# Optimization experiments

Measured on AMD Instinct MI355X. Metric: run time of the kernel, lower is better.

The kernel has to match this reference:

```python
import jax, jax.numpy as jnp
import numpy as np

J6, J3 = 13, 30          # joints with 6-dim and 3-dim outputs (contiguous groups)
J = J6 + J3              # 43 joints total
D = 512                  # latent_dim
B, T = 16, 196


def setup_inputs() -> dict:
    key = jax.random.key(0)
    ks = jax.random.split(key, 7)
    s = 0.02  # weight init scale
    return {
        "x":   jax.random.normal(ks[0], (B, T, J, D), dtype=jnp.float32),
        "W1":  jax.random.normal(ks[1], (J, D, D), dtype=jnp.float32) * s,
        "b1":  jax.random.normal(ks[2], (J, D), dtype=jnp.float32) * s,
        "W2a": jax.random.normal(ks[3], (J6, D, 6), dtype=jnp.float32) * s,
        "b2a": jax.random.normal(ks[4], (J6, 6), dtype=jnp.float32) * s,
        "W2b": jax.random.normal(ks[5], (J3, D, 3), dtype=jnp.float32) * s,
        "b2b": jax.random.normal(ks[6], (J3, 3), dtype=jnp.float32) * s,
    }


def reference(x, W1, b1, W2a, b2a, W2b, b2b):
    # Per-joint MLP: Linear(D,D) -> GELU -> Linear(D,out_dim_j), concatenated
    # over joints along the last dim (heterogeneous 'dk' mode, vectorized).
    h = jnp.einsum('btjd,jde->btje', x, W1) + b1          # [B,T,J,D]
    h = jax.nn.gelu(h, approximate=False)                  # torch nn.GELU (erf)
    oa = jnp.einsum('btjd,jdo->btjo', h[:, :, :J6], W2a) + b2a  # [B,T,13,6]
    ob = jnp.einsum('btjd,jdo->btjo', h[:, :, J6:], W2b) + b2b  # [B,T,30,3]
    b, t = x.shape[0], x.shape[1]
    # torch.cat(out_list, dim=-1) in joint order == group-wise reshape + concat
    motion = jnp.concatenate([oa.reshape(b, t, -1), ob.reshape(b, t, -1)], axis=-1)
    return motion  # [B, T, 13*6 + 30*3] = [B, T, 168]
```

## Files before the change

kernel.cpp:

```cpp
#include <hip/hip_runtime.h>

typedef unsigned short ushort_t;
typedef short short8 __attribute__((ext_vector_type(8)));
typedef float f32x4 __attribute__((ext_vector_type(4)));

#define J_TOT 43
#define J6 13
#define D_DIM 512
#define BT 3136
#define OUTW 168
#define MTILES 49
#define NWG (MTILES * J_TOT)

__device__ __forceinline__ unsigned short bf16rne(float f) {
    unsigned u = __builtin_bit_cast(unsigned, f);
    u += 0x7fffu + ((u >> 16) & 1u);
    return (unsigned short)(u >> 16);
}

__device__ __forceinline__ float gelu_f(float v) {
    float t = v * __builtin_fmaf(v * v, 0.0356774081f, 0.7978845608f);
    float e = __builtin_amdgcn_exp2f(t * 2.8853900818f);
    float s = __builtin_amdgcn_rcpf(1.0f + e);
    return __builtin_fmaf(-v, s, v);
}

__device__ __forceinline__ void async_ld16(const void* gsrc, void* ldst) {
    __builtin_amdgcn_global_load_lds(
        (const __attribute__((address_space(1))) unsigned int*)(unsigned long long)(const char*)gsrc,
        (__attribute__((address_space(3))) unsigned int*)ldst,
        16, 0, 0);
}

__global__ void prepass_kernel(const float* __restrict__ W1, ushort_t* __restrict__ W1t,
                               const float* __restrict__ W2a, const float* __restrict__ b2a,
                               const float* __restrict__ W2b, const float* __restrict__ b2b,
                               ushort_t* __restrict__ W2t, float* __restrict__ b2p) {
    __shared__ __align__(16) ushort_t tile[64][72];
    const int b = blockIdx.x;
    const int t = threadIdx.x;

    if (b < 2752) {
        const int d0 = (b & 7) * 64, e0 = ((b >> 3) & 7) * 64, j = b >> 6;
        const float* src = W1 + (size_t)j * D_DIM * D_DIM;
        const int el = t & 63, dl = t >> 6;
#pragma unroll
        for (int i = 0; i < 16; i++) {
            int d = dl + i * 4;
            tile[el][d] = bf16rne(src[(size_t)(d0 + d) * D_DIM + e0 + el]);
        }
        __syncthreads();
        ushort_t* dst = W1t + (size_t)j * D_DIM * D_DIM;
#pragma unroll
        for (int p = 0; p < 2; p++) {
            int idx = p * 256 + t;
            int e = idx >> 3, c = idx & 7;
            uint4 v = *(const uint4*)(&tile[e][c * 8]);
            *(uint4*)(dst + (size_t)(e0 + e) * D_DIM + d0 + c * 8) = v;
        }
        return;
    }
    const int j = b - 2752;
    const int odim = (j < J6) ? 6 : 3;
    const float* w = (j < J6) ? (W2a + (size_t)j * D_DIM * 6) : (W2b + (size_t)(j - J6) * D_DIM * 3);
    for (int idx = t; idx < 16 * D_DIM; idx += 256) {
        int o = idx >> 9, k = idx & 511;
        float v = (o < odim) ? w[(size_t)k * odim + o] : 0.0f;
        W2t[(size_t)j * 16 * D_DIM + idx] = bf16rne(v);
    }
    if (t < 16) {
        const float* bbv = (j < J6) ? (b2a + (size_t)j * 6) : (b2b + (size_t)(j - J6) * 3);
        b2p[j * 16 + t] = (t < odim) ? bbv[t] : 0.0f;
    }
}

__global__ __launch_bounds__(512, 2)
void MotionDecoder_36309653520632_kernel(const float* __restrict__ x,
                                         const float* __restrict__ b1,
                                         const ushort_t* __restrict__ W1t,
                                         const ushort_t* __restrict__ W2t,
                                         const float* __restrict__ b2p,
                                         float* __restrict__ out) {
    extern __shared__ __align__(16) char smem[];
    char* As = smem;
    char* B0 = smem + 65536;
    char* B1 = smem + 98304;
    char* B2 = smem + 131072;
    char* hs = smem + 65536;

    const int bid = blockIdx.x;
    const int xcd = bid & 7, bi = bid >> 3;
    const int wg = (xcd < 3) ? (xcd * 264 + bi) : (792 + (xcd - 3) * 263 + bi);
    const int j  = wg / MTILES;
    const int mt = wg - j * MTILES;
    const int m0 = mt * 64;

    const int tid  = threadIdx.x;
    const int lane = tid & 63;
    const int w    = tid >> 6;
    const int l15  = lane & 15;
    const int l4   = lane >> 4;

    const ushort_t* w1j = W1t + (size_t)j * D_DIM * D_DIM;

    const ushort_t* bGp0; const ushort_t* bGp1; const ushort_t* bGp2; const ushort_t* bGp3;
    int sB0, sB1, sB2, sB3;
    {
        int rbase = w * 64;
#pragma unroll
        for (int p = 0; p < 4; p++) {
            int rw  = rbase + p * 16;
            int row = rw + (lane >> 2);
            int g   = (lane & 3) ^ ((row >> 1) & 3);
            const ushort_t* gp = w1j + (size_t)row * D_DIM + g * 8;
            int s = rw * 64;
            if (p == 0) { bGp0 = gp; sB0 = s; }
            else if (p == 1) { bGp1 = gp; sB1 = s; }
            else if (p == 2) { bGp2 = gp; sB2 = s; }
            else { bGp3 = gp; sB3 = s; }
        }
    }

#define STAGE_B(buf, kk) do { \
        async_ld16(bGp0 + (kk) * 32, (buf) + sB0); \
        async_ld16(bGp1 + (kk) * 32, (buf) + sB1); \
        async_ld16(bGp2 + (kk) * 32, (buf) + sB2); \
        async_ld16(bGp3 + (kk) * 32, (buf) + sB3); \
    } while (0)

    const int xr = tid >> 3;
    const int c8 = tid & 7;
    const float* xrow = x + ((size_t)(m0 + xr) * J_TOT + j) * D_DIM + c8 * 8;

    float4 xv[16];
#pragma unroll
    for (int i = 0; i < 8; i++) {
        xv[2 * i]     = *(const float4*)(xrow + i * 64);
        xv[2 * i + 1] = *(const float4*)(xrow + i * 64 + 4);
    }
    STAGE_B(B0, 0);
    STAGE_B(B1, 1);
    {
        const int swr = xr & 7;
#pragma unroll
        for (int i = 0; i < 8; i++) {
            union { unsigned short s[8]; uint4 v; } pk;
            float4 f0 = xv[2 * i], f1 = xv[2 * i + 1];
            pk.s[0] = bf16rne(f0.x); pk.s[1] = bf16rne(f0.y);
            pk.s[2] = bf16rne(f0.z); pk.s[3] = bf16rne(f0.w);
            pk.s[4] = bf16rne(f1.x); pk.s[5] = bf16rne(f1.y);
            pk.s[6] = bf16rne(f1.z); pk.s[7] = bf16rne(f1.w);
            int c = c8 + i * 8;
            *(uint4*)(As + xr * 1024 + ((c ^ swr) << 4)) = pk.v;
        }
    }
    float bvv[4];
#pragma unroll
    for (int ct = 0; ct < 4; ct++)
        bvv[ct] = b1[j * D_DIM + w * 64 + ct * 16 + l15];

    asm volatile("s_waitcnt lgkmcnt(0)" ::: "memory");
    __builtin_amdgcn_s_barrier();
    __builtin_amdgcn_sched_barrier(0);

    f32x4 acc[4][4];
#pragma unroll
    for (int a = 0; a < 4; a++)
#pragma unroll
        for (int c = 0; c < 4; c++) acc[a][c] = (f32x4){0.f, 0.f, 0.f, 0.f};

    char* bufA = B0; char* bufB = B1; char* bufC = B2;
    for (int ks = 0; ks < 16; ks++) {
        if (ks < 14) {
            STAGE_B(bufC, ks + 2);
            asm volatile("s_waitcnt vmcnt(8)" ::: "memory");
        } else if (ks == 14) {
            asm volatile("s_waitcnt vmcnt(4)" ::: "memory");
        } else {
            asm volatile("s_waitcnt vmcnt(0)" ::: "memory");
        }
        __builtin_amdgcn_s_barrier();
        __builtin_amdgcn_sched_barrier(0);

        short8 af[4], bf[4];
#pragma unroll
        for (int rt = 0; rt < 4; rt++) {
            int m = rt * 16 + l15;
            int q = ks * 4 + l4;
            af[rt] = *(const short8*)(As + m * 1024 + (((q ^ (m & 7))) << 4));
        }
#pragma unroll
        for (int ct = 0; ct < 4; ct++) {
            int n = w * 64 + ct * 16 + l15;
            bf[ct] = *(const short8*)(bufA + n * 64 + ((l4 ^ ((n >> 1) & 3)) << 4));
        }
        asm volatile("s_waitcnt lgkmcnt(0)" ::: "memory");
        __builtin_amdgcn_s_barrier();
        __builtin_amdgcn_sched_barrier(0);

        __builtin_amdgcn_s_setprio(1);
#pragma unroll
        for (int rt = 0; rt < 4; rt++)
#pragma unroll
            for (int ct = 0; ct < 4; ct++)
                acc[rt][ct] = __builtin_amdgcn_mfma_f32_16x16x32_bf16(
                    af[rt], bf[ct], acc[rt][ct], 0, 0, 0);
        __builtin_amdgcn_s_setprio(0);

        char* tmp = bufA; bufA = bufB; bufB = bufC; bufC = tmp;
    }

#pragma unroll
    for (int ct = 0; ct < 4; ct++) {
        int n = w * 64 + ct * 16 + l15;
        int cc = n >> 3, boff = (n & 7) * 2;
#pragma unroll
        for (int rt = 0; rt < 4; rt++) {
            int mb = rt * 16 + (l4 << 2);
#pragma unroll
            for (int rr = 0; rr < 4; rr++) {
                int m = mb + rr;
                float g = gelu_f(acc[rt][ct][rr] + bvv[ct]);
                *(unsigned short*)(hs + m * 1024 + (((cc ^ (m & 7))) << 4) + boff) = bf16rne(g);
            }
        }
    }
    __syncthreads();

    if (w < 4) {
        const ushort_t* w2j = W2t + (size_t)j * 16 * D_DIM + (size_t)l15 * D_DIM + l4 * 8;
        f32x4 a2acc = (f32x4){0.f, 0.f, 0.f, 0.f};
        const int m = w * 16 + l15;
#pragma unroll
        for (int kc = 0; kc < 16; kc++) {
            short8 wf = *(const short8*)(w2j + kc * 32);
            int q = kc * 4 + l4;
            short8 a2 = *(const short8*)(hs + m * 1024 + (((q ^ (m & 7))) << 4));
            a2acc = __builtin_amdgcn_mfma_f32_16x16x32_bf16(a2, wf, a2acc, 0, 0, 0);
        }
        const int o = l15;
        const int odim = (j < J6) ? 6 : 3;
        const int cb = (j < J6) ? j * 6 : 78 + (j - J6) * 3;
        if (o < odim) {
            float bo = b2p[j * 16 + o];
#pragma unroll
            for (int rr = 0; rr < 4; rr++) {
                int mm = m0 + w * 16 + (l4 << 2) + rr;
                out[(size_t)mm * OUTW + cb + o] = a2acc[rr] + bo;
            }
        }
    }
#undef STAGE_B
}

extern "C" void kernel_launch(void* const* d_in, const int* in_sizes, int n_in,
                              void* d_out, int out_size, void* d_ws, size_t ws_size,
                              hipStream_t stream) {
    const float* x   = (const float*)d_in[0];
    const float* W1  = (const float*)d_in[1];
    const float* b1  = (const float*)d_in[2];
    const float* W2a = (const float*)d_in[3];
    const float* b2a = (const float*)d_in[4];
    const float* W2b = (const float*)d_in[5];
    const float* b2b = (const float*)d_in[6];
    float* out = (float*)d_out;

    ushort_t* W1t = (ushort_t*)d_ws;
    ushort_t* W2t = W1t + (size_t)J_TOT * D_DIM * D_DIM;
    float*    b2p = (float*)(W2t + (size_t)J_TOT * 16 * D_DIM);

    static bool attr_set = false;
    if (!attr_set) {
        (void)hipFuncSetAttribute(
            reinterpret_cast<const void*>(MotionDecoder_36309653520632_kernel),
            hipFuncAttributeMaxDynamicSharedMemorySize, 163840);
        attr_set = true;
    }

    prepass_kernel<<<2752 + J_TOT, 256, 0, stream>>>(W1, W1t, W2a, b2a, W2b, b2b, W2t, b2p);
    MotionDecoder_36309653520632_kernel<<<NWG, 512, 163840, stream>>>(
        x, b1, W1t, W2t, b2p, out);
}
```

Measured before the change: 561.6 us.

## Pre-pack W1 into MFMA fragment order and load it straight to registers

The weight prepass now writes W1 and W2 in per-wave MFMA fragment order, so the main kernel loads weight fragments directly from global memory into registers with a two-deep register double buffer. This removes the LDS staging ring for W1 and its per-step barriers. LDS use drops to 64 KB static and launch bounds rise to allow 4 blocks per CU. The second GEMM is split across all 8 waves with an LDS reduction, and the swizzle changes from XOR to rotate. The cost is that each wave issues its own uncoalesced-in-LDS global loads with no sharing, and the register budget is tighter.

```diff
diff --git a/kernel.cpp b/kernel.cpp
--- a/kernel.cpp
+++ b/kernel.cpp
@@ -25,48 +25,42 @@
     return __builtin_fmaf(-v, s, v);
 }
 
-__device__ __forceinline__ void async_ld16(const void* gsrc, void* ldst) {
-    __builtin_amdgcn_global_load_lds(
-        (const __attribute__((address_space(1))) unsigned int*)(unsigned long long)(const char*)gsrc,
-        (__attribute__((address_space(3))) unsigned int*)ldst,
-        16, 0, 0);
-}
-
-__global__ void prepass_kernel(const float* __restrict__ W1, ushort_t* __restrict__ W1t,
-                               const float* __restrict__ W2a, const float* __restrict__ b2a,
-                               const float* __restrict__ W2b, const float* __restrict__ b2b,
-                               ushort_t* __restrict__ W2t, float* __restrict__ b2p) {
-    __shared__ __align__(16) ushort_t tile[64][72];
+__global__ void pack_kernel(const float* __restrict__ W1, ushort_t* __restrict__ W1f,
+                            const float* __restrict__ W2a, const float* __restrict__ b2a,
+                            const float* __restrict__ W2b, const float* __restrict__ b2b,
+                            ushort_t* __restrict__ W2f, float* __restrict__ b2p) {
     const int b = blockIdx.x;
     const int t = threadIdx.x;
-
-    if (b < 2752) {
-        const int d0 = (b & 7) * 64, e0 = ((b >> 3) & 7) * 64, j = b >> 6;
+    if (b < 5504) {
+        const int j = b >> 7, ks = b & 15, w = (b >> 4) & 7;
+        const int nt = t >> 6, l = t & 63;
         const float* src = W1 + (size_t)j * D_DIM * D_DIM;
-        const int el = t & 63, dl = t >> 6;
-#pragma unroll
-        for (int i = 0; i < 16; i++) {
-            int d = dl + i * 4;
-            tile[el][d] = bf16rne(src[(size_t)(d0 + d) * D_DIM + e0 + el]);
-        }
-        __syncthreads();
-        ushort_t* dst = W1t + (size_t)j * D_DIM * D_DIM;
-#pragma unroll
-        for (int p = 0; p < 2; p++) {
-            int idx = p * 256 + t;
-            int e = idx >> 3, c = idx & 7;
-            uint4 v = *(const uint4*)(&tile[e][c * 8]);
-            *(uint4*)(dst + (size_t)(e0 + e) * D_DIM + d0 + c * 8) = v;
-        }
+        const int k0 = ks * 32 + (l >> 4) * 8;
+        const int n  = w * 64 + nt * 16 + (l & 15);
+        union { unsigned short s[8]; uint4 v; } pk;
+#pragma unroll
+        for (int idx = 0; idx < 8; idx++)
+            pk.s[idx] = bf16rne(src[(size_t)(k0 + idx) * D_DIM + n]);
+        *(uint4*)(W1f + ((size_t)b * 4 + nt) * 512 + (size_t)l * 8) = pk.v;
         return;
     }
-    const int j = b - 2752;
+    const int j = b - 5504;
     const int odim = (j < J6) ? 6 : 3;
-    const float* w = (j < J6) ? (W2a + (size_t)j * D_DIM * 6) : (W2b + (size_t)(j - J6) * D_DIM * 3);
-    for (int idx = t; idx < 16 * D_DIM; idx += 256) {
-        int o = idx >> 9, k = idx & 511;
-        float v = (o < odim) ? w[(size_t)k * odim + o] : 0.0f;
-        W2t[(size_t)j * 16 * D_DIM + idx] = bf16rne(v);
+    const float* wsrc = (j < J6) ? (W2a + (size_t)j * D_DIM * 6)
+                                 : (W2b + (size_t)(j - J6) * D_DIM * 3);
+#pragma unroll
+    for (int p = 0; p < 4; p++) {
+        int ch = p * 256 + t;
+        int l = ch & 63;
+        int n0 = (ch >> 6) * 32 + (l >> 4) * 8;
+        int o  = l & 15;
+        union { unsigned short s[8]; uint4 v; } pk;
+#pragma unroll
+        for (int idx = 0; idx < 8; idx++) {
+            float v = (o < odim) ? wsrc[(size_t)(n0 + idx) * odim + o] : 0.0f;
+            pk.s[idx] = bf16rne(v);
+        }
+        *(uint4*)(W2f + (size_t)j * 8192 + (size_t)ch * 8) = pk.v;
     }
     if (t < 16) {
         const float* bbv = (j < J6) ? (b2a + (size_t)j * 6) : (b2b + (size_t)(j - J6) * 3);
@@ -74,19 +68,14 @@
     }
 }
 
-__global__ __launch_bounds__(512, 2)
+__global__ __launch_bounds__(512, 4)
 void MotionDecoder_36309653520632_kernel(const float* __restrict__ x,
                                          const float* __restrict__ b1,
-                                         const ushort_t* __restrict__ W1t,
-                                         const ushort_t* __restrict__ W2t,
+                                         const ushort_t* __restrict__ W1f,
+                                         const ushort_t* __restrict__ W2f,
                                          const float* __restrict__ b2p,
                                          float* __restrict__ out) {
-    extern __shared__ __align__(16) char smem[];
-    char* As = smem;
-    char* B0 = smem + 65536;
-    char* B1 = smem + 98304;
-    char* B2 = smem + 131072;
-    char* hs = smem + 65536;
+    __shared__ __align__(16) unsigned char smem[65536];
 
     const int bid = blockIdx.x;
     const int xcd = bid & 7, bi = bid >> 3;
@@ -101,67 +90,32 @@
     const int l15  = lane & 15;
     const int l4   = lane >> 4;
 
-    const ushort_t* w1j = W1t + (size_t)j * D_DIM * D_DIM;
-
-    const ushort_t* bGp0; const ushort_t* bGp1; const ushort_t* bGp2; const ushort_t* bGp3;
-    int sB0, sB1, sB2, sB3;
-    {
-        int rbase = w * 64;
-#pragma unroll
-        for (int p = 0; p < 4; p++) {
-            int rw  = rbase + p * 16;
-            int row = rw + (lane >> 2);
-            int g   = (lane & 3) ^ ((row >> 1) & 3);
-            const ushort_t* gp = w1j + (size_t)row * D_DIM + g * 8;
-            int s = rw * 64;
-            if (p == 0) { bGp0 = gp; sB0 = s; }
-            else if (p == 1) { bGp1 = gp; sB1 = s; }
-            else if (p == 2) { bGp2 = gp; sB2 = s; }
-            else { bGp3 = gp; sB3 = s; }
-        }
-    }
-
-#define STAGE_B(buf, kk) do { \
-        async_ld16(bGp0 + (kk) * 32, (buf) + sB0); \
-        async_ld16(bGp1 + (kk) * 32, (buf) + sB1); \
-        async_ld16(bGp2 + (kk) * 32, (buf) + sB2); \
-        async_ld16(bGp3 + (kk) * 32, (buf) + sB3); \
-    } while (0)
-
-    const int xr = tid >> 3;
-    const int c8 = tid & 7;
-    const float* xrow = x + ((size_t)(m0 + xr) * J_TOT + j) * D_DIM + c8 * 8;
-
-    float4 xv[16];
-#pragma unroll
-    for (int i = 0; i < 8; i++) {
-        xv[2 * i]     = *(const float4*)(xrow + i * 64);
-        xv[2 * i + 1] = *(const float4*)(xrow + i * 64 + 4);
-    }
-    STAGE_B(B0, 0);
-    STAGE_B(B1, 1);
-    {
-        const int swr = xr & 7;
-#pragma unroll
-        for (int i = 0; i < 8; i++) {
+    const int xr = tid >> 3, c8 = tid & 7;
+    const float* xrow = x + ((size_t)(m0 + xr) * J_TOT + j) * D_DIM;
+#pragma unroll
+    for (int g = 0; g < 2; g++) {
+        float4 f[8];
+#pragma unroll
+        for (int i = 0; i < 4; i++) {
+            int c = c8 + (g * 4 + i) * 8;
+            f[2 * i]     = *(const float4*)(xrow + c * 8);
+            f[2 * i + 1] = *(const float4*)(xrow + c * 8 + 4);
+        }
+#pragma unroll
+        for (int i = 0; i < 4; i++) {
+            int c = c8 + (g * 4 + i) * 8;
             union { unsigned short s[8]; uint4 v; } pk;
-            float4 f0 = xv[2 * i], f1 = xv[2 * i + 1];
+            float4 f0 = f[2 * i], f1 = f[2 * i + 1];
             pk.s[0] = bf16rne(f0.x); pk.s[1] = bf16rne(f0.y);
             pk.s[2] = bf16rne(f0.z); pk.s[3] = bf16rne(f0.w);
             pk.s[4] = bf16rne(f1.x); pk.s[5] = bf16rne(f1.y);
             pk.s[6] = bf16rne(f1.z); pk.s[7] = bf16rne(f1.w);
-            int c = c8 + i * 8;
-            *(uint4*)(As + xr * 1024 + ((c ^ swr) << 4)) = pk.v;
-        }
-    }
-    float bvv[4];
-#pragma unroll
-    for (int ct = 0; ct < 4; ct++)
-        bvv[ct] = b1[j * D_DIM + w * 64 + ct * 16 + l15];
-
-    asm volatile("s_waitcnt lgkmcnt(0)" ::: "memory");
-    __builtin_amdgcn_s_barrier();
-    __builtin_amdgcn_sched_barrier(0);
+            *(uint4*)(smem + xr * 1024 + (((c + xr) & 63) << 4)) = pk.v;
+        }
+    }
+    __syncthreads();
+
+    const ushort_t* w1f = W1f + ((size_t)j * 8 + w) * 32768 + (size_t)lane * 8;
 
     f32x4 acc[4][4];
 #pragma unroll
@@ -169,75 +123,87 @@
 #pragma unroll
         for (int c = 0; c < 4; c++) acc[a][c] = (f32x4){0.f, 0.f, 0.f, 0.f};
 
-    char* bufA = B0; char* bufB = B1; char* bufC = B2;
-    for (int ks = 0; ks < 16; ks++) {
-        if (ks < 14) {
-            STAGE_B(bufC, ks + 2);
-            asm volatile("s_waitcnt vmcnt(8)" ::: "memory");
-        } else if (ks == 14) {
-            asm volatile("s_waitcnt vmcnt(4)" ::: "memory");
-        } else {
-            asm volatile("s_waitcnt vmcnt(0)" ::: "memory");
-        }
-        __builtin_amdgcn_s_barrier();
-        __builtin_amdgcn_sched_barrier(0);
-
-        short8 af[4], bf[4];
-#pragma unroll
-        for (int rt = 0; rt < 4; rt++) {
-            int m = rt * 16 + l15;
-            int q = ks * 4 + l4;
-            af[rt] = *(const short8*)(As + m * 1024 + (((q ^ (m & 7))) << 4));
-        }
-#pragma unroll
-        for (int ct = 0; ct < 4; ct++) {
-            int n = w * 64 + ct * 16 + l15;
-            bf[ct] = *(const short8*)(bufA + n * 64 + ((l4 ^ ((n >> 1) & 3)) << 4));
-        }
-        asm volatile("s_waitcnt lgkmcnt(0)" ::: "memory");
-        __builtin_amdgcn_s_barrier();
-        __builtin_amdgcn_sched_barrier(0);
-
-        __builtin_amdgcn_s_setprio(1);
-#pragma unroll
-        for (int rt = 0; rt < 4; rt++)
-#pragma unroll
-            for (int ct = 0; ct < 4; ct++)
-                acc[rt][ct] = __builtin_amdgcn_mfma_f32_16x16x32_bf16(
-                    af[rt], bf[ct], acc[rt][ct], 0, 0, 0);
-        __builtin_amdgcn_s_setprio(0);
-
-        char* tmp = bufA; bufA = bufB; bufB = bufC; bufC = tmp;
-    }
-
-#pragma unroll
-    for (int ct = 0; ct < 4; ct++) {
-        int n = w * 64 + ct * 16 + l15;
-        int cc = n >> 3, boff = (n & 7) * 2;
-#pragma unroll
-        for (int rt = 0; rt < 4; rt++) {
-            int mb = rt * 16 + (l4 << 2);
+    short8 awA[4], awB[4];
+#pragma unroll
+    for (int nt = 0; nt < 4; nt++)
+        awA[nt] = *(const short8*)(w1f + nt * 512);
+
+#define K_STEP(CUR, NXT, KS) do {                                              \
+        if ((KS) < 15) {                                                       \
+            _Pragma("unroll")                                                  \
+            for (int nt = 0; nt < 4; nt++)                                     \
+                NXT[nt] = *(const short8*)(w1f + (((KS) + 1) * 4 + nt) * 512); \
+        }                                                                      \
+        short8 bx[4];                                                          \
+        _Pragma("unroll")                                                      \
+        for (int mm = 0; mm < 4; mm++) {                                       \
+            int m = mm * 16 + l15;                                             \
+            bx[mm] = *(const short8*)(smem + m * 1024 +                        \
+                        ((((KS) * 4 + l4 + m) & 63) << 4));                    \
+        }                                                                      \
+        __builtin_amdgcn_s_setprio(1);                                         \
+        _Pragma("unroll")                                                      \
+        for (int nt = 0; nt < 4; nt++)                                         \
+            _Pragma("unroll")                                                  \
+            for (int mm = 0; mm < 4; mm++)                                     \
+                acc[nt][mm] = __builtin_amdgcn_mfma_f32_16x16x32_bf16(         \
+                    CUR[nt], bx[mm], acc[nt][mm], 0, 0, 0);                    \
+        __builtin_amdgcn_s_setprio(0);                                         \
+    } while (0)
+
+#pragma unroll
+    for (int ks2 = 0; ks2 < 8; ks2++) {
+        K_STEP(awA, awB, 2 * ks2);
+        K_STEP(awB, awA, 2 * ks2 + 1);
+    }
+#undef K_STEP
+
+    __syncthreads();
+
+    const float* b1j = b1 + j * D_DIM + w * 64;
+#pragma unroll
+    for (int nt = 0; nt < 4; nt++) {
+        const int nb = nt * 16 + l4 * 4;
+        const int c    = (w * 64 + nb) >> 3;
+        const int half = (nb >> 2) & 1;
+#pragma unroll
+        for (int mm = 0; mm < 4; mm++) {
+            int m = mm * 16 + l15;
+            union { unsigned short s[4]; uint2 v; } pk;
 #pragma unroll
             for (int rr = 0; rr < 4; rr++) {
-                int m = mb + rr;
-                float g = gelu_f(acc[rt][ct][rr] + bvv[ct]);
-                *(unsigned short*)(hs + m * 1024 + (((cc ^ (m & 7))) << 4) + boff) = bf16rne(g);
+                float g = gelu_f(acc[nt][mm][rr] + b1j[nb + rr]);
+                pk.s[rr] = bf16rne(g);
             }
-        }
-    }
-    __syncthreads();
-
+            *(uint2*)(smem + m * 1024 + (((c + m) & 63) << 4) + half * 8) = pk.v;
+        }
+    }
+    __syncthreads();
+
+    const int mt2 = w & 3, kh = w >> 2;
+    const ushort_t* w2f = W2f + (size_t)j * 8192 + (size_t)lane * 8;
+    const int m2 = mt2 * 16 + l15;
+    f32x4 acc2 = (f32x4){0.f, 0.f, 0.f, 0.f};
+#pragma unroll
+    for (int kc2 = 0; kc2 < 8; kc2++) {
+        int kc = kh * 8 + kc2;
+        short8 wfr = *(const short8*)(w2f + kc * 512);
+        int q = kc * 4 + l4;
+        short8 a2 = *(const short8*)(smem + m2 * 1024 + (((q + m2) & 63) << 4));
+        acc2 = __builtin_amdgcn_mfma_f32_16x16x32_bf16(a2, wfr, acc2, 0, 0, 0);
+    }
+    __syncthreads();
+
+    float* red = (float*)smem;
+    if (w >= 4) {
+#pragma unroll
+        for (int rr = 0; rr < 4; rr++) {
+            int mrow = mt2 * 16 + l4 * 4 + rr;
+            red[mrow * 17 + l15] = acc2[rr];
+        }
+    }
+    __syncthreads();
     if (w < 4) {
-        const ushort_t* w2j = W2t + (size_t)j * 16 * D_DIM + (size_t)l15 * D_DIM + l4 * 8;
-        f32x4 a2acc = (f32x4){0.f, 0.f, 0.f, 0.f};
-        const int m = w * 16 + l15;
-#pragma unroll
-        for (int kc = 0; kc < 16; kc++) {
-            short8 wf = *(const short8*)(w2j + kc * 32);
-            int q = kc * 4 + l4;
-            short8 a2 = *(const short8*)(hs + m * 1024 + (((q ^ (m & 7))) << 4));
-            a2acc = __builtin_amdgcn_mfma_f32_16x16x32_bf16(a2, wf, a2acc, 0, 0, 0);
-        }
         const int o = l15;
         const int odim = (j < J6) ? 6 : 3;
         const int cb = (j < J6) ? j * 6 : 78 + (j - J6) * 3;
@@ -245,12 +211,12 @@
             float bo = b2p[j * 16 + o];
 #pragma unroll
             for (int rr = 0; rr < 4; rr++) {
-                int mm = m0 + w * 16 + (l4 << 2) + rr;
-                out[(size_t)mm * OUTW + cb + o] = a2acc[rr] + bo;
+                int mrow = mt2 * 16 + l4 * 4 + rr;
+                float v = acc2[rr] + red[mrow * 17 + l15] + bo;
+                out[(size_t)(m0 + mrow) * OUTW + cb + o] = v;
             }
         }
     }
-#undef STAGE_B
 }
 
 extern "C" void kernel_launch(void* const* d_in, const int* in_sizes, int n_in,
@@ -265,19 +231,11 @@
     const float* b2b = (const float*)d_in[6];
     float* out = (float*)d_out;
 
-    ushort_t* W1t = (ushort_t*)d_ws;
-    ushort_t* W2t = W1t + (size_t)J_TOT * D_DIM * D_DIM;
-    float*    b2p = (float*)(W2t + (size_t)J_TOT * 16 * D_DIM);
-
-    static bool attr_set = false;
-    if (!attr_set) {
-        (void)hipFuncSetAttribute(
-            reinterpret_cast<const void*>(MotionDecoder_36309653520632_kernel),
-            hipFuncAttributeMaxDynamicSharedMemorySize, 163840);
-        attr_set = true;
-    }
-
-    prepass_kernel<<<2752 + J_TOT, 256, 0, stream>>>(W1, W1t, W2a, b2a, W2b, b2b, W2t, b2p);
-    MotionDecoder_36309653520632_kernel<<<NWG, 512, 163840, stream>>>(
-        x, b1, W1t, W2t, b2p, out);
-}
+    ushort_t* W1f = (ushort_t*)d_ws;
+    ushort_t* W2f = W1f + (size_t)J_TOT * D_DIM * D_DIM;
+    float*    b2p = (float*)(W2f + (size_t)J_TOT * 16 * D_DIM);
+
+    pack_kernel<<<5504 + J_TOT, 256, 0, stream>>>(W1, W1f, W2a, b2a, W2b, b2b, W2f, b2p);
+    MotionDecoder_36309653520632_kernel<<<NWG, 512, 0, stream>>>(
+        x, b1, W1f, W2f, b2p, out);
+}
```

Result: faster. 540.5 us (-3.8%).
